# Kernel tuning notes

Hardware: AMD Instinct MI355X
Metric: run time of the kernel (lower is better)

## Reference

```python
import jax, jax.numpy as jnp
import numpy as np

B, S, D, H = 2, 2048, 1024, 16
DK = D // H
SCALE = DK ** 0.5


def setup_inputs() -> dict:
    key = jax.random.key(0)
    ks = jax.random.split(key, 5)
    std = 1.0 / np.sqrt(D)
    return {
        "x": jax.random.normal(ks[0], (B, S, D), dtype=jnp.float32),
        "Wq": jax.random.normal(ks[1], (D, D), dtype=jnp.float32) * std,
        "Wk": jax.random.normal(ks[2], (D, D), dtype=jnp.float32) * std,
        "Wv": jax.random.normal(ks[3], (D, D), dtype=jnp.float32) * std,
        "Wo": jax.random.normal(ks[4], (D, D), dtype=jnp.float32) * std,
    }


def _split_heads(t):
    # [B, S, D] -> [B, H, S, DK]
    b, s, d = t.shape
    return t.reshape(b, s, H, DK).transpose(0, 2, 1, 3)


def reference(x, Wq, Wk, Wv, Wo):
    b, s, d = x.shape
    q = _split_heads(x @ Wq)
    k = _split_heads(x @ Wk)
    v = _split_heads(x @ Wv)
    # scores: [B, H, S, S]
    score = jnp.einsum("bhqd,bhkd->bhqk", q, k)
    causal = jnp.tril(jnp.ones((s, s), dtype=bool))[None, None]
    score = jnp.where(causal, score, -jnp.inf)
    attn = jax.nn.softmax(score / SCALE, axis=-1)
    out = jnp.einsum("bhqk,bhkd->bhqd", attn, v)
    out = out.transpose(0, 2, 1, 3).reshape(b, s, d)
    return out @ Wo
```

## Files before the change

kernel.cpp:

```cpp
#include <hip/hip_runtime.h>
#include <hip/hip_bf16.h>

typedef __bf16 bf16;
typedef __bf16 bf16x8 __attribute__((ext_vector_type(8)));
typedef float f32x4 __attribute__((ext_vector_type(4)));

#define MFMA16(a, b, c) __builtin_amdgcn_mfma_f32_16x16x32_bf16((a), (b), (c), 0, 0, 0)

__device__ __forceinline__ void async16(const void* g, void* l) {
  typedef const unsigned int __attribute__((address_space(1))) * GP;
  typedef unsigned int __attribute__((address_space(3))) * LP;
  __builtin_amdgcn_global_load_lds((GP)g, (LP)l, 16, 0, 0);
}

template <int ctrl>
__device__ __forceinline__ float dppf(float v) {
  return __builtin_bit_cast(
      float, __builtin_amdgcn_update_dpp(0, __builtin_bit_cast(int, v), ctrl,
                                         0xf, 0xf, true));
}
__device__ __forceinline__ float rowsum16(float x) {
  x += dppf<0xB1>(x);
  x += dppf<0x4E>(x);
  x += dppf<0x141>(x);
  x += dppf<0x140>(x);
  return x;
}

__global__ __launch_bounds__(256) void convert_x(
    const float* __restrict__ src, bf16* __restrict__ dst) {
  int i = (blockIdx.x * 256 + threadIdx.x) * 4;
  f32x4 v = *(const f32x4*)&src[i];
  bf16 o[4];
#pragma unroll
  for (int j = 0; j < 4; ++j) o[j] = (bf16)v[j];
  *(ulong1*)&dst[i] = *(ulong1*)o;
}

__global__ __launch_bounds__(256) void transpose_w(
    const float* __restrict__ w0, const float* __restrict__ w1,
    const float* __restrict__ w2, const float* __restrict__ w3,
    bf16* __restrict__ out) {
  __shared__ __align__(16) float tile[64][68];
  const float* src = (blockIdx.z == 0) ? w0 : (blockIdx.z == 1) ? w1
                   : (blockIdx.z == 2) ? w2 : w3;
  bf16* dst = out + (size_t)blockIdx.z * (1024u * 1024u);
  const int t = threadIdx.x;
  const int bx = blockIdx.x, by = blockIdx.y;

#pragma unroll
  for (int p = 0; p < 4; ++p) {
    int idx = t + p * 256;
    int r = idx >> 4, c4 = idx & 15;
    *(f32x4*)&tile[r][c4 * 4] =
        *(const f32x4*)&src[(size_t)(by * 64 + r) * 1024 + bx * 64 + c4 * 4];
  }
  __syncthreads();
#pragma unroll
  for (int p = 0; p < 2; ++p) {
    int idx = t + p * 256;
    int rn = idx >> 3, c8 = idx & 7;
    bf16x8 v;
#pragma unroll
    for (int i = 0; i < 8; ++i) v[i] = (bf16)tile[c8 * 8 + i][rn];
    *(bf16x8*)&dst[(size_t)(bx * 64 + rn) * 1024 + by * 64 + c8 * 8] = v;
  }
}

template <typename OutT, int NI>
__global__ __launch_bounds__(256, 4) void gemm_bt(
    const bf16* __restrict__ A, const bf16* __restrict__ Bt,
    OutT* __restrict__ C, int btStrideZ, int cStrideZ, float scaleZ0,
    bf16* __restrict__ vtOut) {
  const int tid = threadIdx.x;
  const int wave = tid >> 6, lane = tid & 63;
  const int quad = lane >> 4, l16 = lane & 15;
  const int wm = wave >> 1, wn = wave & 1;
  const int m0 = blockIdx.y * 128, n0 = blockIdx.x * (NI * 32);
  const bf16* Bz = Bt + (size_t)blockIdx.z * (size_t)btStrideZ;
  OutT* Cz = C + (size_t)blockIdx.z * (size_t)cStrideZ;
  const float sc = (blockIdx.z == 0) ? scaleZ0 : 1.0f;

  __shared__ __align__(16) bf16 lsA[2][128 * 32];
  __shared__ __align__(16) bf16 lsB[2][NI * 32 * 32];

  const int lrow = lane >> 2;
  const int cgX = (lane & 3) ^ ((lrow >> 1) & 3);
  const int fR = (l16 >> 1) & 3;

  f32x4 acc[4][NI];
#pragma unroll
  for (int i = 0; i < 4; ++i)
#pragma unroll
    for (int j = 0; j < NI; ++j) acc[i][j] = (f32x4){0.f, 0.f, 0.f, 0.f};

#pragma unroll
  for (int c = 0; c < 2; ++c) {
    int chunk = wave * 2 + c;
    int row = chunk * 16 + lrow;
    async16(&A[(size_t)(m0 + row) * 1024 + cgX * 8], &lsA[0][chunk * 512]);
  }
#pragma unroll
  for (int c = 0; c < NI / 2; ++c) {
    int chunk = wave * (NI / 2) + c;
    int row = chunk * 16 + lrow;
    async16(&Bz[(size_t)(n0 + row) * 1024 + cgX * 8], &lsB[0][chunk * 512]);
  }
  __syncthreads();

  for (int it = 0; it < 32; ++it) {
    const int cur = it & 1;
    if (it < 31) {
      int k0n = (it + 1) * 32;
#pragma unroll
      for (int c = 0; c < 2; ++c) {
        int chunk = wave * 2 + c;
        int row = chunk * 16 + lrow;
        async16(&A[(size_t)(m0 + row) * 1024 + k0n + cgX * 8],
                &lsA[cur ^ 1][chunk * 512]);
      }
#pragma unroll
      for (int c = 0; c < NI / 2; ++c) {
        int chunk = wave * (NI / 2) + c;
        int row = chunk * 16 + lrow;
        async16(&Bz[(size_t)(n0 + row) * 1024 + k0n + cgX * 8],
                &lsB[cur ^ 1][chunk * 512]);
      }
    }

    bf16x8 af[4], bfr[NI];
#pragma unroll
    for (int i = 0; i < 4; ++i) {
      int ra = wm * 64 + i * 16 + l16;
      af[i] = *(const bf16x8*)&lsA[cur][ra * 32 + ((quad ^ fR) * 8)];
    }
#pragma unroll
    for (int ni = 0; ni < NI; ++ni) {
      int rb = wn * (NI * 16) + ni * 16 + l16;
      bfr[ni] = *(const bf16x8*)&lsB[cur][rb * 32 + ((quad ^ fR) * 8)];
    }
#pragma unroll
    for (int mi = 0; mi < 4; ++mi)
#pragma unroll
      for (int ni = 0; ni < NI; ++ni)
        acc[mi][ni] = MFMA16(af[mi], bfr[ni], acc[mi][ni]);

    __syncthreads();
  }

  if (blockIdx.z == 2 && vtOut != nullptr) {
#pragma unroll
    for (int mi = 0; mi < 4; ++mi)
#pragma unroll
      for (int ni = 0; ni < NI; ++ni) {
        int col = n0 + wn * (NI * 16) + ni * 16 + l16;
        int h = col >> 6, d = col & 63;
        int row = m0 + wm * 64 + mi * 16 + quad * 4;
        int b = row >> 11, s = row & 2047;
        bf16 o[4];
#pragma unroll
        for (int r = 0; r < 4; ++r) o[r] = (bf16)acc[mi][ni][r];
        *(ulong1*)&vtOut[((size_t)(b * 16 + h) * 64 + d) * 2048 + s] =
            *(ulong1*)o;
      }
  } else {
#pragma unroll
    for (int mi = 0; mi < 4; ++mi)
#pragma unroll
      for (int ni = 0; ni < NI; ++ni) {
        int col = n0 + wn * (NI * 16) + ni * 16 + l16;
#pragma unroll
        for (int r = 0; r < 4; ++r) {
          int row = m0 + wm * 64 + mi * 16 + quad * 4 + r;
          Cz[(size_t)row * 1024 + col] = (OutT)(acc[mi][ni][r] * sc);
        }
      }
  }
}

__global__ __launch_bounds__(512, 4) void attn_fwd(
    const bf16* __restrict__ Q, const bf16* __restrict__ K,
    const bf16* __restrict__ Vt, bf16* __restrict__ O) {
  const int bid = blockIdx.x;
  const int x = bid & 15, hb = bid >> 4;
  const int h = hb & 15, b = hb >> 4;
  const int qt = b ? (15 - x) : x;
  const int tid = threadIdx.x;
  const int wave = tid >> 6, lane = tid & 63;
  const int quad = lane >> 4, l16 = lane & 15;

  __shared__ __align__(16) bf16 QsPs[128 * 64];
  __shared__ __align__(16) bf16 Ks[2][64 * 64];
  __shared__ __align__(16) bf16 Vs[2][64 * 64];

  const size_t base = ((size_t)b * 2048) * 1024 + (size_t)h * 64;
  const bf16* Qb = Q + base;
  const bf16* Kb = K + base;
  const bf16* Vtb = Vt + ((size_t)(b * 16 + h)) * 64 * 2048;
  bf16* Ob = O + base;

  const int lrow = lane >> 3;
  const int cgX = (lane & 7) ^ lrow;

#pragma unroll
  for (int c = 0; c < 2; ++c) {
    int chunk = wave * 2 + c;
    int row = chunk * 8 + lrow;
    async16(&Qb[(size_t)(qt * 128 + row) * 1024 + cgX * 8],
            &QsPs[chunk * 512]);
  }
  {
    int row = wave * 8 + lrow;
    async16(&Kb[(size_t)row * 1024 + cgX * 8], &Ks[0][wave * 512]);
    async16(&Vtb[(size_t)row * 2048 + cgX * 8], &Vs[0][wave * 512]);
  }
  __syncthreads();

  bf16x8 aq[2];
#pragma unroll
  for (int ks = 0; ks < 2; ++ks) {
    int row = wave * 16 + l16;
    aq[ks] =
        *(const bf16x8*)&QsPs[row * 64 + (((ks * 4 + quad) ^ (l16 & 7)) * 8)];
  }

  const float NEG_INF = -__builtin_inff();
  float ls_acc[4] = {0.f, 0.f, 0.f, 0.f};
  f32x4 Oacc[4];
#pragma unroll
  for (int nt = 0; nt < 4; ++nt) Oacc[nt] = (f32x4){0.f, 0.f, 0.f, 0.f};

  bf16* Psp = &QsPs[0];
  const int kt_end = 2 * qt + 1;
  const int ktd = 2 * qt + (wave >> 2);

  for (int kt = 0; kt <= kt_end; ++kt) {
    const int cur = kt & 1;
    if (kt < kt_end) {
      int row = wave * 8 + lrow;
      async16(&Kb[(size_t)((kt + 1) * 64 + row) * 1024 + cgX * 8],
              &Ks[cur ^ 1][wave * 512]);
      async16(&Vtb[(size_t)row * 2048 + (kt + 1) * 64 + cgX * 8],
              &Vs[cur ^ 1][wave * 512]);
    }

    if (kt <= ktd) {
      f32x4 sv[4];
#pragma unroll
      for (int nt = 0; nt < 4; ++nt) {
        int row = nt * 16 + l16;
        bf16x8 bk0 =
            *(const bf16x8*)&Ks[cur][row * 64 + ((quad ^ (l16 & 7)) * 8)];
        bf16x8 bk1 = *(const bf16x8*)&Ks[cur][row * 64 +
                                             (((4 + quad) ^ (l16 & 7)) * 8)];
        sv[nt] = (f32x4){0.f, 0.f, 0.f, 0.f};
        sv[nt] = MFMA16(aq[0], bk0, sv[nt]);
        sv[nt] = MFMA16(aq[1], bk1, sv[nt]);
      }

      if (kt == ktd) {
        const int rowb = wave * 16 + quad * 4;
        const int cb = (kt - 2 * qt) * 64;
#pragma unroll
        for (int nt = 0; nt < 4; ++nt) {
          const int col = cb + nt * 16 + l16;
#pragma unroll
          for (int r = 0; r < 4; ++r)
            if (col > rowb + r) sv[nt][r] = NEG_INF;
        }
      }
#pragma unroll
      for (int nt = 0; nt < 4; ++nt)
#pragma unroll
        for (int r = 0; r < 4; ++r) {
          float p = exp2f(sv[nt][r]);
          sv[nt][r] = p;
          ls_acc[r] += p;
        }

#pragma unroll
      for (int nt = 0; nt < 4; ++nt) {
        const int col = nt * 16 + l16;
        const int cg = col >> 3;
#pragma unroll
        for (int r = 0; r < 4; ++r) {
          int prow = wave * 16 + quad * 4 + r;
          Psp[prow * 64 + ((cg ^ (prow & 7)) * 8) + (col & 7)] =
              (bf16)sv[nt][r];
        }
      }

      const int arow = wave * 16 + l16;
      bf16x8 ap0 = *(const bf16x8*)&Psp[arow * 64 + ((quad ^ (l16 & 7)) * 8)];
      bf16x8 ap1 =
          *(const bf16x8*)&Psp[arow * 64 + (((4 + quad) ^ (l16 & 7)) * 8)];
#pragma unroll
      for (int nt = 0; nt < 4; ++nt) {
        int row = nt * 16 + l16;
        bf16x8 bv0 =
            *(const bf16x8*)&Vs[cur][row * 64 + ((quad ^ (l16 & 7)) * 8)];
        bf16x8 bv1 = *(const bf16x8*)&Vs[cur][row * 64 +
                                             (((4 + quad) ^ (l16 & 7)) * 8)];
        Oacc[nt] = MFMA16(ap0, bv0, Oacc[nt]);
        Oacc[nt] = MFMA16(ap1, bv1, Oacc[nt]);
      }
    }

    __syncthreads();
  }

  float rl[4];
#pragma unroll
  for (int r = 0; r < 4; ++r) rl[r] = 1.f / rowsum16(ls_acc[r]);
#pragma unroll
  for (int nt = 0; nt < 4; ++nt)
#pragma unroll
    for (int r = 0; r < 4; ++r) {
      int row = qt * 128 + wave * 16 + quad * 4 + r;
      Ob[(size_t)row * 1024 + nt * 16 + l16] = (bf16)(Oacc[nt][r] * rl[r]);
    }
}

extern "C" void kernel_launch(void* const* d_in, const int* in_sizes, int n_in,
                              void* d_out, int out_size, void* d_ws,
                              size_t ws_size, hipStream_t stream) {
  (void)in_sizes; (void)n_in; (void)out_size; (void)ws_size;
  const float* x  = (const float*)d_in[0];
  const float* Wq = (const float*)d_in[1];
  const float* Wk = (const float*)d_in[2];
  const float* Wv = (const float*)d_in[3];
  const float* Wo = (const float*)d_in[4];
  float* out = (float*)d_out;

  bf16* ws = (bf16*)d_ws;
  const size_t WELEM = 1024u * 1024u;
  const size_t TELEM = 4096u * 1024u;
  bf16* wt  = ws;
  bf16* xbf = ws + 4 * WELEM;
  bf16* q   = xbf + TELEM;
  bf16* k   = q + TELEM;
  bf16* vt  = k + TELEM;
  bf16* ao  = vt + TELEM;

  const float QSCALE = 0.125f * 1.44269504088896340736f;

  convert_x<<<dim3(4096), 256, 0, stream>>>(x, xbf);
  transpose_w<<<dim3(16, 16, 4), 256, 0, stream>>>(Wq, Wk, Wv, Wo, wt);
  gemm_bt<bf16, 2><<<dim3(16, 32, 3), 256, 0, stream>>>(
      xbf, wt, q, (int)WELEM, (int)TELEM, QSCALE, vt);
  attn_fwd<<<dim3(512), 512, 0, stream>>>(q, k, vt, ao);
  gemm_bt<float, 2><<<dim3(16, 32, 1), 256, 0, stream>>>(
      ao, wt + 3 * WELEM, out, 0, 0, 1.0f, nullptr);
}
```

Measured before the change: 198.3 us.

## Keep P in registers via transposed QK MFMA and merge prep kernels

The QK^T MFMA operands are swapped so each lane holds a column of scores. The exponentiated probabilities can then feed the PV MFMA directly from registers, which removes the P round-trip through shared memory. V is read as two 4-element halves to match the new operand layout, and the row-sum reduction becomes cross-quad shuffles. Shared memory is merged into one 32KB buffer, with Q overlapping the second K/V stage, and an extra barrier is added after the Q load. The x conversion and weight transpose are also fused into a single launch to save one kernel launch.

```diff
diff --git a/kernel.cpp b/kernel.cpp
--- a/kernel.cpp
+++ b/kernel.cpp
@@ -2,6 +2,7 @@
 #include <hip/hip_bf16.h>
 
 typedef __bf16 bf16;
+typedef __bf16 bf16x4 __attribute__((ext_vector_type(4)));
 typedef __bf16 bf16x8 __attribute__((ext_vector_type(8)));
 typedef float f32x4 __attribute__((ext_vector_type(4)));
 
@@ -13,41 +14,30 @@
   __builtin_amdgcn_global_load_lds((GP)g, (LP)l, 16, 0, 0);
 }
 
-template <int ctrl>
-__device__ __forceinline__ float dppf(float v) {
-  return __builtin_bit_cast(
-      float, __builtin_amdgcn_update_dpp(0, __builtin_bit_cast(int, v), ctrl,
-                                         0xf, 0xf, true));
-}
-__device__ __forceinline__ float rowsum16(float x) {
-  x += dppf<0xB1>(x);
-  x += dppf<0x4E>(x);
-  x += dppf<0x141>(x);
-  x += dppf<0x140>(x);
-  return x;
-}
-
-__global__ __launch_bounds__(256) void convert_x(
-    const float* __restrict__ src, bf16* __restrict__ dst) {
-  int i = (blockIdx.x * 256 + threadIdx.x) * 4;
-  f32x4 v = *(const f32x4*)&src[i];
-  bf16 o[4];
-#pragma unroll
-  for (int j = 0; j < 4; ++j) o[j] = (bf16)v[j];
-  *(ulong1*)&dst[i] = *(ulong1*)o;
-}
-
-__global__ __launch_bounds__(256) void transpose_w(
+__global__ __launch_bounds__(256) void prep(
     const float* __restrict__ w0, const float* __restrict__ w1,
     const float* __restrict__ w2, const float* __restrict__ w3,
-    bf16* __restrict__ out) {
+    const float* __restrict__ x, bf16* __restrict__ wtOut,
+    bf16* __restrict__ xOut) {
+  const int t = threadIdx.x;
+  if (blockIdx.z == 4) {
+    size_t base = ((size_t)(blockIdx.y * 16 + blockIdx.x)) * 16384;
+#pragma unroll
+    for (int p = 0; p < 16; ++p) {
+      size_t i = base + (size_t)(p * 256 + t) * 4;
+      f32x4 v = *(const f32x4*)&x[i];
+      bf16 o[4];
+#pragma unroll
+      for (int j = 0; j < 4; ++j) o[j] = (bf16)v[j];
+      *(ulong1*)&xOut[i] = *(ulong1*)o;
+    }
+    return;
+  }
   __shared__ __align__(16) float tile[64][68];
   const float* src = (blockIdx.z == 0) ? w0 : (blockIdx.z == 1) ? w1
                    : (blockIdx.z == 2) ? w2 : w3;
-  bf16* dst = out + (size_t)blockIdx.z * (1024u * 1024u);
-  const int t = threadIdx.x;
+  bf16* dst = wtOut + (size_t)blockIdx.z * (1024u * 1024u);
   const int bx = blockIdx.x, by = blockIdx.y;
-
 #pragma unroll
   for (int p = 0; p < 4; ++p) {
     int idx = t + p * 256;
@@ -189,9 +179,10 @@
   const int wave = tid >> 6, lane = tid & 63;
   const int quad = lane >> 4, l16 = lane & 15;
 
-  __shared__ __align__(16) bf16 QsPs[128 * 64];
-  __shared__ __align__(16) bf16 Ks[2][64 * 64];
-  __shared__ __align__(16) bf16 Vs[2][64 * 64];
+  __shared__ __align__(16) bf16 SMEM[16384];
+  const int kof[2] = {0, 8192};
+  const int vof[2] = {4096, 12288};
+  bf16* Qs = &SMEM[8192];
 
   const size_t base = ((size_t)b * 2048) * 1024 + (size_t)h * 64;
   const bf16* Qb = Q + base;
@@ -206,13 +197,12 @@
   for (int c = 0; c < 2; ++c) {
     int chunk = wave * 2 + c;
     int row = chunk * 8 + lrow;
-    async16(&Qb[(size_t)(qt * 128 + row) * 1024 + cgX * 8],
-            &QsPs[chunk * 512]);
+    async16(&Qb[(size_t)(qt * 128 + row) * 1024 + cgX * 8], &Qs[chunk * 512]);
   }
   {
     int row = wave * 8 + lrow;
-    async16(&Kb[(size_t)row * 1024 + cgX * 8], &Ks[0][wave * 512]);
-    async16(&Vtb[(size_t)row * 2048 + cgX * 8], &Vs[0][wave * 512]);
+    async16(&Kb[(size_t)row * 1024 + cgX * 8], &SMEM[kof[0] + wave * 512]);
+    async16(&Vtb[(size_t)row * 2048 + cgX * 8], &SMEM[vof[0] + wave * 512]);
   }
   __syncthreads();
 
@@ -220,17 +210,16 @@
 #pragma unroll
   for (int ks = 0; ks < 2; ++ks) {
     int row = wave * 16 + l16;
-    aq[ks] =
-        *(const bf16x8*)&QsPs[row * 64 + (((ks * 4 + quad) ^ (l16 & 7)) * 8)];
-  }
+    aq[ks] = *(const bf16x8*)&Qs[row * 64 + (((ks * 4 + quad) ^ (l16 & 7)) * 8)];
+  }
+  __syncthreads();
 
   const float NEG_INF = -__builtin_inff();
-  float ls_acc[4] = {0.f, 0.f, 0.f, 0.f};
+  float ls_acc = 0.f;
   f32x4 Oacc[4];
 #pragma unroll
   for (int nt = 0; nt < 4; ++nt) Oacc[nt] = (f32x4){0.f, 0.f, 0.f, 0.f};
 
-  bf16* Psp = &QsPs[0];
   const int kt_end = 2 * qt + 1;
   const int ktd = 2 * qt + (wave >> 2);
 
@@ -239,9 +228,9 @@
     if (kt < kt_end) {
       int row = wave * 8 + lrow;
       async16(&Kb[(size_t)((kt + 1) * 64 + row) * 1024 + cgX * 8],
-              &Ks[cur ^ 1][wave * 512]);
+              &SMEM[kof[cur ^ 1] + wave * 512]);
       async16(&Vtb[(size_t)row * 2048 + (kt + 1) * 64 + cgX * 8],
-              &Vs[cur ^ 1][wave * 512]);
+              &SMEM[vof[cur ^ 1] + wave * 512]);
     }
 
     if (kt <= ktd) {
@@ -249,69 +238,70 @@
 #pragma unroll
       for (int nt = 0; nt < 4; ++nt) {
         int row = nt * 16 + l16;
-        bf16x8 bk0 =
-            *(const bf16x8*)&Ks[cur][row * 64 + ((quad ^ (l16 & 7)) * 8)];
-        bf16x8 bk1 = *(const bf16x8*)&Ks[cur][row * 64 +
-                                             (((4 + quad) ^ (l16 & 7)) * 8)];
+        bf16x8 bk0 = *(const bf16x8*)&SMEM[kof[cur] + row * 64 +
+                                           ((quad ^ (l16 & 7)) * 8)];
+        bf16x8 bk1 = *(const bf16x8*)&SMEM[kof[cur] + row * 64 +
+                                           (((4 + quad) ^ (l16 & 7)) * 8)];
         sv[nt] = (f32x4){0.f, 0.f, 0.f, 0.f};
-        sv[nt] = MFMA16(aq[0], bk0, sv[nt]);
-        sv[nt] = MFMA16(aq[1], bk1, sv[nt]);
+        sv[nt] = MFMA16(bk0, aq[0], sv[nt]);
+        sv[nt] = MFMA16(bk1, aq[1], sv[nt]);
       }
 
       if (kt == ktd) {
-        const int rowb = wave * 16 + quad * 4;
+        const int q_rel = wave * 16 + l16;
         const int cb = (kt - 2 * qt) * 64;
 #pragma unroll
         for (int nt = 0; nt < 4; ++nt) {
-          const int col = cb + nt * 16 + l16;
+          const int kb = cb + nt * 16 + quad * 4;
 #pragma unroll
           for (int r = 0; r < 4; ++r)
-            if (col > rowb + r) sv[nt][r] = NEG_INF;
+            if (kb + r > q_rel) sv[nt][r] = NEG_INF;
         }
       }
-#pragma unroll
-      for (int nt = 0; nt < 4; ++nt)
-#pragma unroll
-        for (int r = 0; r < 4; ++r) {
-          float p = exp2f(sv[nt][r]);
-          sv[nt][r] = p;
-          ls_acc[r] += p;
+
+      bf16x8 apf[2];
+#pragma unroll
+      for (int a = 0; a < 2; ++a)
+#pragma unroll
+        for (int g = 0; g < 2; ++g)
+#pragma unroll
+          for (int r = 0; r < 4; ++r) {
+            float p = exp2f(sv[a * 2 + g][r]);
+            ls_acc += p;
+            apf[a][g * 4 + r] = (bf16)p;
+          }
+
+#pragma unroll
+      for (int nt = 0; nt < 4; ++nt) {
+        const int R = nt * 16 + l16;
+        const int sub = (quad & 1) * 4;
+#pragma unroll
+        for (int a = 0; a < 2; ++a) {
+          const int g0 = a * 4 + (quad >> 1);
+          const int g1 = g0 + 2;
+          bf16x4 lo = *(const bf16x4*)&SMEM[vof[cur] + R * 64 +
+                                            ((g0 ^ (l16 & 7)) * 8) + sub];
+          bf16x4 hi = *(const bf16x4*)&SMEM[vof[cur] + R * 64 +
+                                            ((g1 ^ (l16 & 7)) * 8) + sub];
+          bf16x8 bvf;
+#pragma unroll
+          for (int i = 0; i < 4; ++i) {
+            bvf[i] = lo[i];
+            bvf[4 + i] = hi[i];
+          }
+          Oacc[nt] = MFMA16(apf[a], bvf, Oacc[nt]);
         }
-
-#pragma unroll
-      for (int nt = 0; nt < 4; ++nt) {
-        const int col = nt * 16 + l16;
-        const int cg = col >> 3;
-#pragma unroll
-        for (int r = 0; r < 4; ++r) {
-          int prow = wave * 16 + quad * 4 + r;
-          Psp[prow * 64 + ((cg ^ (prow & 7)) * 8) + (col & 7)] =
-              (bf16)sv[nt][r];
-        }
-      }
-
-      const int arow = wave * 16 + l16;
-      bf16x8 ap0 = *(const bf16x8*)&Psp[arow * 64 + ((quad ^ (l16 & 7)) * 8)];
-      bf16x8 ap1 =
-          *(const bf16x8*)&Psp[arow * 64 + (((4 + quad) ^ (l16 & 7)) * 8)];
-#pragma unroll
-      for (int nt = 0; nt < 4; ++nt) {
-        int row = nt * 16 + l16;
-        bf16x8 bv0 =
-            *(const bf16x8*)&Vs[cur][row * 64 + ((quad ^ (l16 & 7)) * 8)];
-        bf16x8 bv1 = *(const bf16x8*)&Vs[cur][row * 64 +
-                                             (((4 + quad) ^ (l16 & 7)) * 8)];
-        Oacc[nt] = MFMA16(ap0, bv0, Oacc[nt]);
-        Oacc[nt] = MFMA16(ap1, bv1, Oacc[nt]);
       }
     }
 
     __syncthreads();
   }
 
+  ls_acc += __shfl_xor(ls_acc, 16, 64);
+  ls_acc += __shfl_xor(ls_acc, 32, 64);
   float rl[4];
 #pragma unroll
-  for (int r = 0; r < 4; ++r) rl[r] = 1.f / rowsum16(ls_acc[r]);
+  for (int r = 0; r < 4; ++r) rl[r] = 1.f / __shfl(ls_acc, quad * 4 + r, 64);
 #pragma unroll
   for (int nt = 0; nt < 4; ++nt)
 #pragma unroll
@@ -344,8 +334,7 @@
 
   const float QSCALE = 0.125f * 1.44269504088896340736f;
 
-  convert_x<<<dim3(4096), 256, 0, stream>>>(x, xbf);
-  transpose_w<<<dim3(16, 16, 4), 256, 0, stream>>>(Wq, Wk, Wv, Wo, wt);
+  prep<<<dim3(16, 16, 5), 256, 0, stream>>>(Wq, Wk, Wv, Wo, x, wt, xbf);
   gemm_bt<bf16, 2><<<dim3(16, 32, 3), 256, 0, stream>>>(
       xbf, wt, q, (int)WELEM, (int)TELEM, QSCALE, vt);
   attn_fwd<<<dim3(512), 512, 0, stream>>>(q, k, vt, ao);
```

Result: faster. 190.6 us (-3.9%).
